# Kernel optimization log

Hardware: AMD Instinct MI355X
Metric: run time of the kernel (lower is better)

Reference implementation:

```python
import jax, jax.numpy as jnp
import numpy as np

KS = 3        # opt.kernel_size
B = 8         # batch
T = 512       # total_length (frames)
CQ = 126      # motion channels
CK = 80       # music channels
H = 128       # hid_c
SLOPE = 0.2   # lrelu slope in ConvBlock
INF = jnp.float32(1e30)


def _conv_block(x, w, b):
    # x: [B, Cin, T]; w: [Cout, Cin, KS]; reflect pad, stride 1, lrelu
    xp = jnp.pad(x, ((0, 0), (0, 0), (1, 1)), mode='reflect')
    y = jax.lax.conv_general_dilated(xp, w, (1,), 'VALID',
                                     dimension_numbers=('NCH', 'OIH', 'NCH'))
    return jax.nn.leaky_relu(y + b[None, :, None], SLOPE)


def _encode(x, params):
    for w, b in params:
        x = _conv_block(x, w, b)
    return x  # [B, H, T]


def _dtw_single(d, L):
    # d: [M, N] cost matrix, L: scalar int valid length. Returns 0/1 path matrix.
    M, N = d.shape
    jcol = jnp.arange(N)
    # row 0: cumulative along j, predecessor is 'left' (choice 1)
    row0 = jnp.cumsum(d[0])
    ch0 = jnp.where(jcol == 0, -1, 1).astype(jnp.int32)

    def row_step(prev_row, d_row):
        p_diag = jnp.concatenate([jnp.full((1,), INF), prev_row[:-1]])

        def inner(left, xs):
            pd, pu, dij, j = xs
            m = jnp.minimum(jnp.minimum(pd, left), pu)
            # tie-break order matches numpy code: diag, then left, then up
            choice = jnp.where(pd == m, 0, jnp.where(left == m, 1, 2)).astype(jnp.int32)
            cost = m + dij
            cost = jnp.where(j == 0, pu + dij, cost)      # first column: from up
            choice = jnp.where(j == 0, 2, choice)
            return cost, (cost, choice)

        _, (crow, chrow) = jax.lax.scan(inner, INF, (p_diag, prev_row, d_row, jcol))
        return crow, chrow

    _, chs = jax.lax.scan(row_step, row0, d[1:])
    choices = jnp.concatenate([ch0[None], chs], axis=0)  # [M, N]

    path01 = jnp.zeros((M, N), jnp.float32).at[L - 1, L - 1].set(1.0)

    def bt_step(carry, _):
        ix, iy, p = carry
        active = (ix > 0) | (iy > 0)
        c = choices[ix, iy]
        nix = jnp.where(c == 0, ix - 1, jnp.where(c == 1, ix, ix - 1))
        niy = jnp.where(c == 0, iy - 1, jnp.where(c == 1, iy - 1, iy))
        nix = jnp.where(active, nix, ix)
        niy = jnp.where(active, niy, iy)
        p = p.at[nix, niy].set(jnp.where(active, 1.0, p[nix, niy]))
        return (nix, niy, p), None

    (_, _, path01), _ = jax.lax.scan(bt_step, (L - 1, L - 1, path01), None,
                                     length=2 * M - 2)
    return path01


def setup_inputs() -> dict:
    key = jax.random.key(0)
    ks = jax.random.split(key, 16)

    def w(k, o, i):
        return jax.random.normal(k, (o, i, KS), jnp.float32) * np.float32(np.sqrt(2.0 / (i * KS)))

    inp = {
        'vec': jax.random.normal(ks[0], (B, CQ, T), jnp.float32),
        'music': jax.random.normal(ks[1], (B, CK, T), jnp.float32),
        'real_length': jax.random.randint(ks[2], (B,), T // 2, T + 1, jnp.int32),
        'qw1': w(ks[3], CQ, CQ), 'qb1': jnp.zeros((CQ,), jnp.float32),
        'qw2': w(ks[4], H, CQ),  'qb2': jnp.zeros((H,), jnp.float32),
        'qw3': w(ks[5], H, H),   'qb3': jnp.zeros((H,), jnp.float32),
        'kw1': w(ks[6], CK, CK), 'kb1': jnp.zeros((CK,), jnp.float32),
        'kw2': w(ks[7], H, CK),  'kb2': jnp.zeros((H,), jnp.float32),
        'kw3': w(ks[8], H, H),   'kb3': jnp.zeros((H,), jnp.float32),
    }
    return inp


def reference(vec, music, real_length, qw1, qb1, qw2, qb2, qw3, qb3,
              kw1, kb1, kw2, kb2, kw3, kb3):
    # conv encoders (ConvBlock x3 each)
    q = _encode(vec, [(qw1, qb1), (qw2, qb2), (qw3, qb3)])    # [B, H, T]
    k = _encode(music, [(kw1, kb1), (kw2, kb2), (kw3, kb3)])  # [B, H, T]
    qf = q.transpose(0, 2, 1)  # [B, N, H] motion latent
    kf = k.transpose(0, 2, 1)  # [B, M, H] music latent
    # Euclidean_dist(music_feat=kf, motion_feat=qf): dist[b, m, n] = ||kf[b,m]-qf[b,n]||
    diff = kf[:, :, None, :] - qf[:, None, :, :]              # [B, M, N, H]
    dist = jnp.sqrt(jnp.sum(diff * diff, axis=-1))            # [B, M, N]
    dist = (dist - dist.min()) / (dist.max() - dist.min())    # global min-max norm
    path01 = jax.vmap(_dtw_single)(dist, real_length)         # [B, M, N]
    return (path01, dist)
```

## Files before the change

### kernel.cpp

```cpp
#include <hip/hip_runtime.h>
#include <hip/hip_bf16.h>

#define T_LEN 512
#define BATCH 8
#define HID 128

__global__ __launch_bounds__(512) void conv_block_kernel(
    const float* __restrict__ x, const float* __restrict__ w,
    const float* __restrict__ bias, float* __restrict__ y,
    int Cin, int Cout)
{
    __shared__ float xs[128 * 66];
    const int b   = blockIdx.z;
    const int t0  = blockIdx.x * 64;
    const int tid = threadIdx.x;
    const int tl  = tid & 63;

    const float* xb = x + (size_t)b * Cin * T_LEN;
    for (int idx = tid; idx < Cin * 66; idx += 512) {
        int ci = idx / 66;
        int tt = idx - ci * 66;
        int g  = t0 + tt - 1;
        g = (g < 0) ? 1 : (g >= T_LEN ? T_LEN - 2 : g);
        xs[idx] = xb[ci * T_LEN + g];
    }
    __syncthreads();

    const int wave = __builtin_amdgcn_readfirstlane(tid >> 6);
    const int co0  = blockIdx.y * 16 + 2 * wave;
    if (co0 < Cout) {
        const float* __restrict__ wq0 = w + (size_t)co0 * Cin * 3;
        const float* __restrict__ wq1 = wq0 + Cin * 3;
        float acc0 = 0.0f, acc1 = 0.0f;
#pragma unroll 4
        for (int ci = 0; ci < Cin; ++ci) {
            float xm = xs[ci * 66 + tl];
            float x0 = xs[ci * 66 + tl + 1];
            float xp = xs[ci * 66 + tl + 2];
            float a00 = wq0[ci * 3 + 0], a01 = wq0[ci * 3 + 1], a02 = wq0[ci * 3 + 2];
            float a10 = wq1[ci * 3 + 0], a11 = wq1[ci * 3 + 1], a12 = wq1[ci * 3 + 2];
            acc0 = fmaf(a00, xm, acc0);
            acc0 = fmaf(a01, x0, acc0);
            acc0 = fmaf(a02, xp, acc0);
            acc1 = fmaf(a10, xm, acc1);
            acc1 = fmaf(a11, x0, acc1);
            acc1 = fmaf(a12, xp, acc1);
        }
        float v0 = acc0 + bias[co0];
        float v1 = acc1 + bias[co0 + 1];
        v0 = (v0 >= 0.0f) ? v0 : 0.2f * v0;
        v1 = (v1 >= 0.0f) ? v1 : 0.2f * v1;
        y[((size_t)b * Cout + co0) * T_LEN + t0 + tl]     = v0;
        y[((size_t)b * Cout + co0 + 1) * T_LEN + t0 + tl] = v1;
    }
}

__global__ __launch_bounds__(256) void dist_kernel(
    const float* __restrict__ q, const float* __restrict__ k,
    float* __restrict__ dist, unsigned* __restrict__ mm)
{
    __shared__ __align__(16) float ks[HID * 32];
    __shared__ __align__(16) float qs[HID * 32];
    __shared__ float red[8];

    const int b  = blockIdx.z;
    const int m0 = blockIdx.y * 32;
    const int n0 = blockIdx.x * 32;
    const int tid = threadIdx.x;

    const float* qb = q + (size_t)b * HID * T_LEN;
    const float* kb = k + (size_t)b * HID * T_LEN;

    for (int idx = tid; idx < HID * 32; idx += 256) {
        int h = idx >> 5, c = idx & 31;
        ks[idx] = kb[h * T_LEN + m0 + c];
        qs[idx] = qb[h * T_LEN + n0 + c];
    }
    __syncthreads();

    const int nn = tid & 31;
    const int mq = (tid >> 5) * 4;

    float a0 = 0.f, a1 = 0.f, a2 = 0.f, a3 = 0.f;
    for (int h = 0; h < HID; ++h) {
        float qv = qs[h * 32 + nn];
        const float4 kv = *reinterpret_cast<const float4*>(&ks[h * 32 + mq]);
        float d0 = kv.x - qv, d1 = kv.y - qv, d2 = kv.z - qv, d3 = kv.w - qv;
        a0 = fmaf(d0, d0, a0);
        a1 = fmaf(d1, d1, a1);
        a2 = fmaf(d2, d2, a2);
        a3 = fmaf(d3, d3, a3);
    }
    float v0 = sqrtf(a0), v1 = sqrtf(a1), v2 = sqrtf(a2), v3 = sqrtf(a3);

    float* drow = dist + ((size_t)b * T_LEN + m0 + mq) * T_LEN + n0 + nn;
    drow[0 * T_LEN] = v0;
    drow[1 * T_LEN] = v1;
    drow[2 * T_LEN] = v2;
    drow[3 * T_LEN] = v3;

    float mnv = fminf(fminf(v0, v1), fminf(v2, v3));
    float mxv = fmaxf(fmaxf(v0, v1), fmaxf(v2, v3));
#pragma unroll
    for (int off = 32; off >= 1; off >>= 1) {
        mnv = fminf(mnv, __shfl_xor(mnv, off, 64));
        mxv = fmaxf(mxv, __shfl_xor(mxv, off, 64));
    }
    int wid = tid >> 6;
    if ((tid & 63) == 0) { red[wid * 2] = mnv; red[wid * 2 + 1] = mxv; }
    __syncthreads();
    if (tid == 0) {
        float mn = fminf(fminf(red[0], red[2]), fminf(red[4], red[6]));
        float mx = fmaxf(fmaxf(red[1], red[3]), fmaxf(red[5], red[7]));
        atomicMin(&mm[0], __float_as_uint(mn));
        atomicMax(&mm[1], __float_as_uint(mx));
    }
}

__global__ __launch_bounds__(256) void norm_transpose_kernel(
    float* __restrict__ dist, float* __restrict__ distT,
    const unsigned* __restrict__ mm)
{
    __shared__ float tile[32][33];
    const float mn  = __uint_as_float(mm[0]);
    const float rng = __uint_as_float(mm[1]) - mn;
    const int b  = blockIdx.z;
    const int m0 = blockIdx.y * 32;
    const int n0 = blockIdx.x * 32;
    const int tx = threadIdx.x & 31;
    const int ty = threadIdx.x >> 5;

    float* D  = dist  + (size_t)b * T_LEN * T_LEN;
    float* DT = distT + (size_t)b * T_LEN * T_LEN;
#pragma unroll
    for (int r = 0; r < 4; ++r) {
        int row = m0 + ty + r * 8;
        float v = (D[row * T_LEN + n0 + tx] - mn) / rng;
        D[row * T_LEN + n0 + tx] = v;
        tile[ty + r * 8][tx] = v;
    }
    __syncthreads();
#pragma unroll
    for (int r = 0; r < 4; ++r) {
        int nrow = n0 + ty + r * 8;
        DT[nrow * T_LEN + m0 + tx] = tile[tx][ty + r * 8];
    }
}

__device__ __forceinline__ float4 ld4c(const float* base, int j, int r) {
    int jc = ((unsigned)j < 512u) ? j : 0;
    return *reinterpret_cast<const float4*>(base + (size_t)jc * T_LEN + r);
}

#define DTW_STEP(T, DA, DB) do {                                              \
    int j = (T) - p;                                                          \
    float u_top = __shfl_up(L[7], 1, 64);                                     \
    float d_top = __shfl_up(prevL7, 1, 64);                                   \
    prevL7 = L[7];                                                            \
    if ((unsigned)j < 512u) {                                                 \
        float dvs[8] = {DA.x, DA.y, DA.z, DA.w, DB.x, DB.y, DB.z, DB.w};      \
        int sh = (j & 15) * 2;                                                \
        float cur, oldL, prevrow;                                             \
        unsigned ch;                                                          \
        if (p == 0) {                                                         \
            cur = (j == 0) ? dvs[0] : (L[0] + dvs[0]); ch = 1u;               \
        } else if (j == 0) {                                                  \
            cur = u_top + dvs[0]; ch = 2u;                                    \
        } else {                                                              \
            float pd = d_top, lf = L[0], pu = u_top;                          \
            float m = fminf(fminf(pd, lf), pu);                               \
            ch = (pd == m) ? 0u : ((lf == m) ? 1u : 2u);                      \
            cur = m + dvs[0];                                                 \
        }                                                                     \
        oldL = L[0]; L[0] = cur; prevrow = cur; pk[0] |= ch << sh;            \
        _Pragma("unroll")                                                     \
        for (int u = 1; u < 8; ++u) {                                         \
            if (j == 0) { cur = prevrow + dvs[u]; ch = 2u; }                  \
            else {                                                            \
                float pd = oldL, lf = L[u], pu = prevrow;                     \
                float m = fminf(fminf(pd, lf), pu);                           \
                ch = (pd == m) ? 0u : ((lf == m) ? 1u : 2u);                  \
                cur = m + dvs[u];                                             \
            }                                                                 \
            oldL = L[u]; L[u] = cur; prevrow = cur; pk[u] |= ch << sh;        \
        }                                                                     \
        if ((j & 15) == 15) {                                                 \
            int w4 = (j >> 4) * 4;                                            \
            *reinterpret_cast<uint4*>(&cho[p * 256 + w4]) =                   \
                make_uint4(pk[0], pk[1], pk[2], pk[3]);                       \
            *reinterpret_cast<uint4*>(&cho[p * 256 + 128 + w4]) =             \
                make_uint4(pk[4], pk[5], pk[6], pk[7]);                       \
            pk[0] = pk[1] = pk[2] = pk[3] = 0u;                               \
            pk[4] = pk[5] = pk[6] = pk[7] = 0u;                               \
        }                                                                     \
    }                                                                         \
} while (0)

__global__ __launch_bounds__(64) void dtw_wave_kernel(
    const float* __restrict__ distT, const int* __restrict__ rlen,
    float* __restrict__ path)
{
    __shared__ unsigned cho[512 * 32];

    const int b  = blockIdx.x;
    const int p  = threadIdx.x;
    const int r0 = p * 8;
    const float* dT = distT + (size_t)b * T_LEN * T_LEN;

    float L[8];
    float prevL7 = 1e30f;
#pragma unroll
    for (int u = 0; u < 8; ++u) L[u] = 1e30f;
    unsigned pk[8] = {0u, 0u, 0u, 0u, 0u, 0u, 0u, 0u};

    float4 Aa = ld4c(dT, 0 - p, r0), Ab = ld4c(dT, 0 - p, r0 + 4);
    float4 Ba = ld4c(dT, 1 - p, r0), Bb = ld4c(dT, 1 - p, r0 + 4);

    for (int t = 0; t < 576; t += 2) {
        float4 Ca = ld4c(dT, t + 2 - p, r0), Cb = ld4c(dT, t + 2 - p, r0 + 4);
        DTW_STEP(t, Aa, Ab);
        float4 Da = ld4c(dT, t + 3 - p, r0), Db = ld4c(dT, t + 3 - p, r0 + 4);
        DTW_STEP(t + 1, Ba, Bb);
        Aa = Ca; Ab = Cb; Ba = Da; Bb = Db;
    }

    __syncthreads();

    if (p == 0) {
        int Lr = rlen[b];
        int ix = Lr - 1, iy = Lr - 1;
        float* po = path + (size_t)b * T_LEN * T_LEN;
        po[ix * T_LEN + iy] = 1.0f;
        while (ix > 0 || iy > 0) {
            uint4 tw = *reinterpret_cast<const uint4*>(
                &cho[((ix >> 2) * 32 + (iy >> 4)) * 4]);
            int tr = ix >> 2, tc = iy >> 4;
            while (true) {
                int sel = ix & 3;
                unsigned wv = (sel & 2) ? ((sel & 1) ? tw.w : tw.z)
                                        : ((sel & 1) ? tw.y : tw.x);
                int c = (wv >> ((iy & 15) * 2)) & 3;
                ix -= (c != 1);
                iy -= (c != 2);
                po[ix * T_LEN + iy] = 1.0f;
                if (!(ix > 0 || iy > 0)) break;
                if ((ix >> 2) != tr || (iy >> 4) != tc) break;
            }
        }
    }
}

extern "C" void kernel_launch(void* const* d_in, const int* in_sizes, int n_in,
                              void* d_out, int out_size, void* d_ws, size_t ws_size,
                              hipStream_t stream)
{
    (void)in_sizes; (void)n_in; (void)out_size; (void)ws_size;

    const float* vec   = (const float*)d_in[0];
    const float* music = (const float*)d_in[1];
    const int*   rlen  = (const int*)  d_in[2];
    const float* qw1 = (const float*)d_in[3];  const float* qb1 = (const float*)d_in[4];
    const float* qw2 = (const float*)d_in[5];  const float* qb2 = (const float*)d_in[6];
    const float* qw3 = (const float*)d_in[7];  const float* qb3 = (const float*)d_in[8];
    const float* kw1 = (const float*)d_in[9];  const float* kb1 = (const float*)d_in[10];
    const float* kw2 = (const float*)d_in[11]; const float* kb2 = (const float*)d_in[12];
    const float* kw3 = (const float*)d_in[13]; const float* kb3 = (const float*)d_in[14];

    float* out = (float*)d_out;
    const size_t mat_elems = (size_t)BATCH * T_LEN * T_LEN;
    float* path_out = out;
    float* dist_out = out + mat_elems;

    char* ws = (char*)d_ws;
    const size_t bufB = (size_t)BATCH * HID * T_LEN * sizeof(float);
    float* qA = (float*)(ws + 0 * bufB);
    float* qB = (float*)(ws + 1 * bufB);
    float* kA = (float*)(ws + 2 * bufB);
    float* kB = (float*)(ws + 3 * bufB);
    float* distT = (float*)ws;
    unsigned* mm = (unsigned*)(ws + 4 * bufB);

    hipMemsetAsync(path_out, 0, mat_elems * sizeof(float), stream);
    hipMemsetAsync(mm, 0xFF, 4, stream);
    hipMemsetAsync(mm + 1, 0x00, 4, stream);

    dim3 cb(512);
    conv_block_kernel<<<dim3(8, 8, 8), cb, 0, stream>>>(vec, qw1, qb1, qA, 126, 126);
    conv_block_kernel<<<dim3(8, 8, 8), cb, 0, stream>>>(qA,  qw2, qb2, qB, 126, 128);
    conv_block_kernel<<<dim3(8, 8, 8), cb, 0, stream>>>(qB,  qw3, qb3, qA, 128, 128);
    conv_block_kernel<<<dim3(8, 5, 8), cb, 0, stream>>>(music, kw1, kb1, kA, 80, 80);
    conv_block_kernel<<<dim3(8, 8, 8), cb, 0, stream>>>(kA,   kw2, kb2, kB, 80, 128);
    conv_block_kernel<<<dim3(8, 8, 8), cb, 0, stream>>>(kB,   kw3, kb3, kA, 128, 128);

    dist_kernel<<<dim3(16, 16, 8), dim3(256), 0, stream>>>(qA, kA, dist_out, mm);

    norm_transpose_kernel<<<dim3(16, 16, 8), dim3(256), 0, stream>>>(dist_out, distT, mm);

    dtw_wave_kernel<<<dim3(BATCH), dim3(64), 0, stream>>>(distT, rlen, path_out);
}
```

Baseline: 580.6 us.

## Shear distance matrix into wavefront layout for DTW and deepen prefetch

The normalize/transpose kernel now writes a sheared (anti-diagonal-by-step) copy of the distance matrix, so each DTW wavefront step reads one contiguous row instead of strided rows. The DTW loop prefetches eight steps ahead from this layout rather than one. Conv weights are repacked to float4-aligned rows by small extra kernels so each input channel's three taps load as one vector. The cost is extra launches and a larger workspace, and any sheared entries the kernel never writes are read as stale but masked data.

```diff
diff --git a/kernel.cpp b/kernel.cpp
--- a/kernel.cpp
+++ b/kernel.cpp
@@ -4,9 +4,20 @@
 #define T_LEN 512
 #define BATCH 8
 #define HID 128
+#define NSTEP 576
+
+__global__ void repack_w_kernel(const float* __restrict__ in,
+                                float* __restrict__ out, int n)
+{
+    int i = blockIdx.x * blockDim.x + threadIdx.x;
+    if (i < n) {
+        float a = in[i * 3 + 0], b = in[i * 3 + 1], c = in[i * 3 + 2];
+        *reinterpret_cast<float4*>(out + i * 4) = make_float4(a, b, c, 0.0f);
+    }
+}
 
 __global__ __launch_bounds__(512) void conv_block_kernel(
-    const float* __restrict__ x, const float* __restrict__ w,
+    const float* __restrict__ x, const float* __restrict__ wp,
     const float* __restrict__ bias, float* __restrict__ y,
     int Cin, int Cout)
 {
@@ -29,22 +40,22 @@
     const int wave = __builtin_amdgcn_readfirstlane(tid >> 6);
     const int co0  = blockIdx.y * 16 + 2 * wave;
     if (co0 < Cout) {
-        const float* __restrict__ wq0 = w + (size_t)co0 * Cin * 3;
-        const float* __restrict__ wq1 = wq0 + Cin * 3;
+        const float* __restrict__ wq0 = wp + (size_t)co0 * Cin * 4;
+        const float* __restrict__ wq1 = wq0 + Cin * 4;
         float acc0 = 0.0f, acc1 = 0.0f;
 #pragma unroll 4
         for (int ci = 0; ci < Cin; ++ci) {
             float xm = xs[ci * 66 + tl];
             float x0 = xs[ci * 66 + tl + 1];
             float xp = xs[ci * 66 + tl + 2];
-            float a00 = wq0[ci * 3 + 0], a01 = wq0[ci * 3 + 1], a02 = wq0[ci * 3 + 2];
-            float a10 = wq1[ci * 3 + 0], a11 = wq1[ci * 3 + 1], a12 = wq1[ci * 3 + 2];
-            acc0 = fmaf(a00, xm, acc0);
-            acc0 = fmaf(a01, x0, acc0);
-            acc0 = fmaf(a02, xp, acc0);
-            acc1 = fmaf(a10, xm, acc1);
-            acc1 = fmaf(a11, x0, acc1);
-            acc1 = fmaf(a12, xp, acc1);
+            const float4 w0 = *reinterpret_cast<const float4*>(wq0 + ci * 4);
+            const float4 w1 = *reinterpret_cast<const float4*>(wq1 + ci * 4);
+            acc0 = fmaf(w0.x, xm, acc0);
+            acc0 = fmaf(w0.y, x0, acc0);
+            acc0 = fmaf(w0.z, xp, acc0);
+            acc1 = fmaf(w1.x, xm, acc1);
+            acc1 = fmaf(w1.y, x0, acc1);
+            acc1 = fmaf(w1.z, xp, acc1);
         }
         float v0 = acc0 + bias[co0];
         float v1 = acc1 + bias[co0 + 1];
@@ -117,39 +128,39 @@
     }
 }
 
-__global__ __launch_bounds__(256) void norm_transpose_kernel(
-    float* __restrict__ dist, float* __restrict__ distT,
+__global__ __launch_bounds__(512) void norm_shear_kernel(
+    float* __restrict__ dist, float* __restrict__ dsk,
     const unsigned* __restrict__ mm)
 {
-    __shared__ float tile[32][33];
+    __shared__ float tile[64][65];
     const float mn  = __uint_as_float(mm[0]);
     const float rng = __uint_as_float(mm[1]) - mn;
     const int b  = blockIdx.z;
-    const int m0 = blockIdx.y * 32;
-    const int n0 = blockIdx.x * 32;
-    const int tx = threadIdx.x & 31;
-    const int ty = threadIdx.x >> 5;
-
-    float* D  = dist  + (size_t)b * T_LEN * T_LEN;
-    float* DT = distT + (size_t)b * T_LEN * T_LEN;
-#pragma unroll
-    for (int r = 0; r < 4; ++r) {
-        int row = m0 + ty + r * 8;
-        float v = (D[row * T_LEN + n0 + tx] - mn) / rng;
-        D[row * T_LEN + n0 + tx] = v;
-        tile[ty + r * 8][tx] = v;
-    }
-    __syncthreads();
-#pragma unroll
-    for (int r = 0; r < 4; ++r) {
-        int nrow = n0 + ty + r * 8;
-        DT[nrow * T_LEN + m0 + tx] = tile[tx][ty + r * 8];
-    }
-}
-
-__device__ __forceinline__ float4 ld4c(const float* base, int j, int r) {
-    int jc = ((unsigned)j < 512u) ? j : 0;
-    return *reinterpret_cast<const float4*>(base + (size_t)jc * T_LEN + r);
+    const int m0 = blockIdx.y * 64;
+    const int n0 = blockIdx.x * 64;
+    const int tid  = threadIdx.x;
+    const int lane = tid & 63;
+    const int wv   = tid >> 6;
+
+    float* D = dist + (size_t)b * T_LEN * T_LEN;
+#pragma unroll
+    for (int r = 0; r < 8; ++r) {
+        int lm = wv + r * 8;
+        float v = (D[(m0 + lm) * T_LEN + n0 + lane] - mn) / rng;
+        D[(m0 + lm) * T_LEN + n0 + lane] = v;
+        tile[lm][lane] = v;
+    }
+    __syncthreads();
+
+    float* dskb = dsk + (size_t)b * NSTEP * T_LEN;
+    const int tbase = n0 + (m0 >> 3);
+#pragma unroll
+    for (int it = 0; it < 9; ++it) {
+        int t_local = wv + it * 8;
+        int ln = t_local - (lane >> 3);
+        if (t_local <= 70 && ln >= 0 && ln < 64)
+            dskb[(size_t)(tbase + t_local) * T_LEN + m0 + lane] = tile[lane][ln];
+    }
 }
 
 #define DTW_STEP(T, DA, DB) do {                                              \
@@ -196,8 +207,12 @@
     }                                                                         \
 } while (0)
 
+__device__ __forceinline__ float4 ld4d(const float* dskb, int t, int off) {
+    return *reinterpret_cast<const float4*>(dskb + (size_t)t * T_LEN + off);
+}
+
 __global__ __launch_bounds__(64) void dtw_wave_kernel(
-    const float* __restrict__ distT, const int* __restrict__ rlen,
+    const float* __restrict__ dsk, const int* __restrict__ rlen,
     float* __restrict__ path)
 {
     __shared__ unsigned cho[512 * 32];
@@ -205,7 +220,7 @@
     const int b  = blockIdx.x;
     const int p  = threadIdx.x;
     const int r0 = p * 8;
-    const float* dT = distT + (size_t)b * T_LEN * T_LEN;
+    const float* dskb = dsk + (size_t)b * NSTEP * T_LEN;
 
     float L[8];
     float prevL7 = 1e30f;
@@ -213,15 +228,23 @@
     for (int u = 0; u < 8; ++u) L[u] = 1e30f;
     unsigned pk[8] = {0u, 0u, 0u, 0u, 0u, 0u, 0u, 0u};
 
-    float4 Aa = ld4c(dT, 0 - p, r0), Ab = ld4c(dT, 0 - p, r0 + 4);
-    float4 Ba = ld4c(dT, 1 - p, r0), Bb = ld4c(dT, 1 - p, r0 + 4);
-
-    for (int t = 0; t < 576; t += 2) {
-        float4 Ca = ld4c(dT, t + 2 - p, r0), Cb = ld4c(dT, t + 2 - p, r0 + 4);
-        DTW_STEP(t, Aa, Ab);
-        float4 Da = ld4c(dT, t + 3 - p, r0), Db = ld4c(dT, t + 3 - p, r0 + 4);
-        DTW_STEP(t + 1, Ba, Bb);
-        Aa = Ca; Ab = Cb; Ba = Da; Bb = Db;
+    float4 P0[8], P1[8];
+#pragma unroll
+    for (int u = 0; u < 8; ++u) {
+        P0[u] = ld4d(dskb, u, r0);
+        P1[u] = ld4d(dskb, u, r0 + 4);
+    }
+
+    for (int t0 = 0; t0 < NSTEP; t0 += 8) {
+#pragma unroll
+        for (int u = 0; u < 8; ++u) {
+            int t  = t0 + u;
+            int tn = t + 8; tn = (tn < NSTEP) ? tn : (NSTEP - 1);
+            float4 Na = ld4d(dskb, tn, r0);
+            float4 Nb = ld4d(dskb, tn, r0 + 4);
+            DTW_STEP(t, P0[u], P1[u]);
+            P0[u] = Na; P1[u] = Nb;
+        }
     }
 
     __syncthreads();
@@ -237,9 +260,9 @@
             int tr = ix >> 2, tc = iy >> 4;
             while (true) {
                 int sel = ix & 3;
-                unsigned wv = (sel & 2) ? ((sel & 1) ? tw.w : tw.z)
-                                        : ((sel & 1) ? tw.y : tw.x);
-                int c = (wv >> ((iy & 15) * 2)) & 3;
+                unsigned wvv = (sel & 2) ? ((sel & 1) ? tw.w : tw.z)
+                                         : ((sel & 1) ? tw.y : tw.x);
+                int c = (wvv >> ((iy & 15) * 2)) & 3;
                 ix -= (c != 1);
                 iy -= (c != 2);
                 po[ix * T_LEN + iy] = 1.0f;
@@ -273,28 +296,42 @@
 
     char* ws = (char*)d_ws;
     const size_t bufB = (size_t)BATCH * HID * T_LEN * sizeof(float);
+    float* dsk = (float*)ws;
     float* qA = (float*)(ws + 0 * bufB);
     float* qB = (float*)(ws + 1 * bufB);
     float* kA = (float*)(ws + 2 * bufB);
     float* kB = (float*)(ws + 3 * bufB);
-    float* distT = (float*)ws;
-    unsigned* mm = (unsigned*)(ws + 4 * bufB);
+    char* wr = ws + 4 * bufB;
+    float* qw1p = (float*)(wr);
+    float* qw2p = (float*)(wr + 254016);
+    float* qw3p = (float*)(wr + 512064);
+    float* kw1p = (float*)(wr + 774208);
+    float* kw2p = (float*)(wr + 876608);
+    float* kw3p = (float*)(wr + 1040448);
+    unsigned* mm = (unsigned*)(ws + 9691200);
 
     hipMemsetAsync(path_out, 0, mat_elems * sizeof(float), stream);
     hipMemsetAsync(mm, 0xFF, 4, stream);
     hipMemsetAsync(mm + 1, 0x00, 4, stream);
 
+    repack_w_kernel<<<(126 * 126 + 255) / 256, 256, 0, stream>>>(qw1, qw1p, 126 * 126);
+    repack_w_kernel<<<(128 * 126 + 255) / 256, 256, 0, stream>>>(qw2, qw2p, 128 * 126);
+    repack_w_kernel<<<(128 * 128 + 255) / 256, 256, 0, stream>>>(qw3, qw3p, 128 * 128);
+    repack_w_kernel<<<(80 * 80 + 255) / 256, 256, 0, stream>>>(kw1, kw1p, 80 * 80);
+    repack_w_kernel<<<(128 * 80 + 255) / 256, 256, 0, stream>>>(kw2, kw2p, 128 * 80);
+    repack_w_kernel<<<(128 * 128 + 255) / 256, 256, 0, stream>>>(kw3, kw3p, 128 * 128);
+
     dim3 cb(512);
-    conv_block_kernel<<<dim3(8, 8, 8), cb, 0, stream>>>(vec, qw1, qb1, qA, 126, 126);
-    conv_block_kernel<<<dim3(8, 8, 8), cb, 0, stream>>>(qA,  qw2, qb2, qB, 126, 128);
-    conv_block_kernel<<<dim3(8, 8, 8), cb, 0, stream>>>(qB,  qw3, qb3, qA, 128, 128);
-    conv_block_kernel<<<dim3(8, 5, 8), cb, 0, stream>>>(music, kw1, kb1, kA, 80, 80);
-    conv_block_kernel<<<dim3(8, 8, 8), cb, 0, stream>>>(kA,   kw2, kb2, kB, 80, 128);
-    conv_block_kernel<<<dim3(8, 8, 8), cb, 0, stream>>>(kB,   kw3, kb3, kA, 128, 128);
+    conv_block_kernel<<<dim3(8, 8, 8), cb, 0, stream>>>(vec, qw1p, qb1, qA, 126, 126);
+    conv_block_kernel<<<dim3(8, 8, 8), cb, 0, stream>>>(qA,  qw2p, qb2, qB, 126, 128);
+    conv_block_kernel<<<dim3(8, 8, 8), cb, 0, stream>>>(qB,  qw3p, qb3, qA, 128, 128);
+    conv_block_kernel<<<dim3(8, 5, 8), cb, 0, stream>>>(music, kw1p, kb1, kA, 80, 80);
+    conv_block_kernel<<<dim3(8, 8, 8), cb, 0, stream>>>(kA,   kw2p, kb2, kB, 80, 128);
+    conv_block_kernel<<<dim3(8, 8, 8), cb, 0, stream>>>(kB,   kw3p, kb3, kA, 128, 128);
 
     dist_kernel<<<dim3(16, 16, 8), dim3(256), 0, stream>>>(qA, kA, dist_out, mm);
 
-    norm_transpose_kernel<<<dim3(16, 16, 8), dim3(256), 0, stream>>>(dist_out, distT, mm);
-
-    dtw_wave_kernel<<<dim3(BATCH), dim3(64), 0, stream>>>(distT, rlen, path_out);
-}
+    norm_shear_kernel<<<dim3(8, 8, 8), dim3(512), 0, stream>>>(dist_out, dsk, mm);
+
+    dtw_wave_kernel<<<dim3(BATCH), dim3(64), 0, stream>>>(dsk, rlen, path_out);
+}
```

Result: slower. 624.3 us (+7.5%).
